# Kernel tuning notes

Hardware: AMD Instinct MI355X
Metric: run time of the kernel (lower is better)

## Reference

```python
import jax, jax.numpy as jnp
import numpy as np

B, S, E, H, R = 8, 1024, 768, 12, 16

def setup_inputs() -> dict:
    key = jax.random.key(0)
    ks = jax.random.split(key, 9)
    sc = 0.02
    return {
        "q": jax.random.normal(ks[0], (B, S, E), jnp.float32),
        "k": jax.random.normal(ks[1], (B, S, E), jnp.float32),
        "v": jax.random.normal(ks[2], (B, S, E), jnp.float32),
        "in_proj_weight": jax.random.normal(ks[3], (3 * E, E), jnp.float32) * sc,
        "in_proj_bias": jax.random.normal(ks[4], (3 * E,), jnp.float32) * sc,
        "out_w": jax.random.normal(ks[5], (E, E), jnp.float32) * sc,
        "out_b": jax.random.normal(ks[6], (E,), jnp.float32) * sc,
        "lora_a": jax.random.normal(ks[7], (R, E), jnp.float32) * sc,
        "lora_b": jax.random.normal(ks[8], (3 * E, R), jnp.float32) * sc,
        "num_heads": H,
    }

def _heads(x, h):
    b, s, e = x.shape
    return x.reshape(b, s, h, e // h).transpose(0, 2, 1, 3)  # [B,H,S,D]

def reference(q, k, v, in_proj_weight, in_proj_bias, out_w, out_b, lora_a, lora_b, num_heads):
    e = q.shape[-1]
    hd = e // num_heads
    scaling = float(hd) ** -0.5
    wq, wk, wv = in_proj_weight[:e], in_proj_weight[e:2 * e], in_proj_weight[2 * e:]
    bq, bk, bv = in_proj_bias[:e], in_proj_bias[e:2 * e], in_proj_bias[2 * e:]
    # base projections + LoRA delta (x @ A^T @ B_slice^T)
    qh = _heads(q @ wq.T + bq + (q @ lora_a.T) @ lora_b[:e].T, num_heads)
    kh = _heads(k @ wk.T + bk + (k @ lora_a.T) @ lora_b[e:2 * e].T, num_heads)
    vh = _heads(v @ wv.T + bv + (v @ lora_a.T) @ lora_b[2 * e:].T, num_heads)
    qh = qh * scaling
    attn = jax.nn.softmax(jnp.einsum('bhqd,bhkd->bhqk', qh, kh), axis=-1)
    out = jnp.einsum('bhqk,bhkd->bhqd', attn, vh)  # [B,H,S,D]
    out = out.transpose(0, 2, 1, 3).reshape(q.shape[0], q.shape[1], e)
    return out @ out_w.T + out_b
```

## Files before the change

kernel.cpp:

```cpp
#include <hip/hip_runtime.h>
#include <hip/hip_bf16.h>


typedef __attribute__((ext_vector_type(4))) float f32x4;
typedef __attribute__((ext_vector_type(16))) float f32x16;
typedef __attribute__((ext_vector_type(8))) short bf16x8;
typedef __attribute__((ext_vector_type(4))) short s16x4;

#define E_DIM 768
#define NB 8
#define SEQ 1024
#define NH 12
#define HD 64
#define M_DIM (NB * SEQ)

__device__ __forceinline__ short f2b(float f) {
    union { __hip_bfloat16 h; short s; } u;
    u.h = __float2bfloat16(f);
    return u.s;
}

__device__ __forceinline__ void async_cp16(const void* g, void* l) {
    __builtin_amdgcn_global_load_lds(
        (const __attribute__((address_space(1))) void*)g,
        (__attribute__((address_space(3))) void*)l, 16, 0, 0);
}


__global__ void cvt_qkv_kernel(const float* __restrict__ q, const float* __restrict__ k,
                               const float* __restrict__ v, short* __restrict__ dst) {
    const float* src = (blockIdx.y == 0) ? q : (blockIdx.y == 1 ? k : v);
    short* out = dst + (size_t)blockIdx.y * (size_t)(M_DIM * E_DIM);
    size_t i = ((size_t)blockIdx.x * 256 + threadIdx.x) * 8;
    float4 a = *(const float4*)(src + i);
    float4 b = *(const float4*)(src + i + 4);
    bf16x8 o;
    o[0] = f2b(a.x); o[1] = f2b(a.y); o[2] = f2b(a.z); o[3] = f2b(a.w);
    o[4] = f2b(b.x); o[5] = f2b(b.y); o[6] = f2b(b.z); o[7] = f2b(b.w);
    *(bf16x8*)(out + i) = o;
}

__global__ void weff_kernel(const float* __restrict__ ipw, const float* __restrict__ la,
                            const float* __restrict__ lb, short* __restrict__ W) {
    int idx = blockIdx.x * 256 + threadIdx.x;
    int r = idx / 192;
    int c = (idx % 192) * 4;
    float4 acc = *(const float4*)(ipw + (size_t)r * E_DIM + c);
    #pragma unroll
    for (int j = 0; j < 16; ++j) {
        float bb = lb[r * 16 + j];
        float4 aa = *(const float4*)(la + j * E_DIM + c);
        acc.x += bb * aa.x; acc.y += bb * aa.y; acc.z += bb * aa.z; acc.w += bb * aa.w;
    }
    s16x4 o; o[0] = f2b(acc.x); o[1] = f2b(acc.y); o[2] = f2b(acc.z); o[3] = f2b(acc.w);
    *(s16x4*)(W + (size_t)r * E_DIM + c) = o;
}

__global__ void cvt_w_kernel(const float* __restrict__ w, short* __restrict__ out) {
    int i = (blockIdx.x * 256 + threadIdx.x) * 4;
    float4 a = *(const float4*)(w + i);
    s16x4 o; o[0] = f2b(a.x); o[1] = f2b(a.y); o[2] = f2b(a.z); o[3] = f2b(a.w);
    *(s16x4*)(out + i) = o;
}

template <int MODE>
__global__ __launch_bounds__(256) void gemm_bt(
    const short* __restrict__ Aall, const short* __restrict__ Ball,
    const float* __restrict__ biasAll,
    short* __restrict__ Qb, short* __restrict__ Kb, short* __restrict__ Vt,
    float* __restrict__ Cout) {
    __shared__ short sA[128 * 64];
    __shared__ short sB[128 * 64];
    const int z = blockIdx.z;
    const short* Ap = Aall + (size_t)z * (size_t)(M_DIM * E_DIM);
    const short* Bp = Ball + (size_t)z * (size_t)(E_DIM * E_DIM);
    const float* bias = biasAll + z * E_DIM;
    const int tm = blockIdx.x * 128;
    const int tn = blockIdx.y * 128;
    const int t = threadIdx.x;
    const int lane = t & 63, wid = t >> 6;
    const int wr = wid >> 1, wc = wid & 1;
    const int lr = lane & 15, lg = lane >> 4;
    const int srow = lane >> 3;
    const int sgrp = lane & 7;

    f32x4 acc[4][4] = {};

    for (int k0 = 0; k0 < E_DIM; k0 += 64) {
        #pragma unroll
        for (int is = 0; is < 4; ++is) {
            const int rbase = is * 32 + wid * 8;
            const int row = rbase + srow;
            const int gsw = (sgrp ^ (row & 7)) << 3;
            async_cp16(Ap + (size_t)(tm + row) * E_DIM + k0 + gsw, &sA[rbase * 64]);
            async_cp16(Bp + (size_t)(tn + row) * E_DIM + k0 + gsw, &sB[rbase * 64]);
        }
        __syncthreads();
        #pragma unroll
        for (int kk = 0; kk < 2; ++kk) {
            bf16x8 af[4], bfr[4];
            const int kg = kk * 4 + lg;
            #pragma unroll
            for (int i = 0; i < 4; ++i) {
                const int row = wr * 64 + i * 16 + lr;
                af[i] = *(const bf16x8*)&sA[row * 64 + ((kg ^ (row & 7)) << 3)];
            }
            #pragma unroll
            for (int j = 0; j < 4; ++j) {
                const int col = wc * 64 + j * 16 + lr;
                bfr[j] = *(const bf16x8*)&sB[col * 64 + ((kg ^ (col & 7)) << 3)];
            }
            #pragma unroll
            for (int i = 0; i < 4; ++i)
                #pragma unroll
                for (int j = 0; j < 4; ++j)
                    acc[i][j] = __builtin_amdgcn_mfma_f32_16x16x32_bf16(
                        af[i], bfr[j], acc[i][j], 0, 0, 0);
        }
        __syncthreads();
    }

    #pragma unroll
    for (int i = 0; i < 4; ++i) {
        const int m0 = tm + wr * 64 + i * 16 + lg * 4;
        const int b = m0 >> 10;
        const int s0 = m0 & 1023;
        #pragma unroll
        for (int j = 0; j < 4; ++j) {
            const int n = tn + wc * 64 + j * 16 + lr;
            const float bia = bias[n];
            f32x4 a = acc[i][j];
            if (MODE == 1) {
                #pragma unroll
                for (int r = 0; r < 4; ++r)
                    Cout[(size_t)(m0 + r) * E_DIM + n] = a[r] + bia;
            } else {
                const int h = n >> 6, d = n & 63;
                const int bh = b * NH + h;
                if (z == 0) {
                    #pragma unroll
                    for (int r = 0; r < 4; ++r)
                        Qb[((size_t)bh * SEQ + s0 + r) * HD + d] = f2b((a[r] + bia) * 0.125f);
                } else if (z == 1) {
                    #pragma unroll
                    for (int r = 0; r < 4; ++r)
                        Kb[((size_t)bh * SEQ + s0 + r) * HD + d] = f2b(a[r] + bia);
                } else {
                    s16x4 pk;
                    #pragma unroll
                    for (int r = 0; r < 4; ++r) pk[r] = f2b(a[r] + bia);
                    *(s16x4*)&Vt[((size_t)bh * HD + d) * SEQ + s0] = pk;
                }
            }
        }
    }
}

__global__ __launch_bounds__(256) void attn_kernel(
    const short* __restrict__ Qb, const short* __restrict__ Kb,
    const short* __restrict__ Vt, short* __restrict__ Ob) {
    __shared__ short sK[2][32 * HD];
    __shared__ short sV[2][HD * 32];

    const int t = threadIdx.x;
    const int lane = t & 63, wid = t >> 6;
    const int l31 = lane & 31, hi = lane >> 5;

    const int p = blockIdx.x;
    const int bh = (p & 7) * 12 + ((p >> 3) >> 3);
    const int qblk = (p >> 3) & 7;
    const int q0 = qblk * 128 + wid * 32;

    const short* Qp = Qb + (size_t)bh * (SEQ * HD);
    const short* Kp = Kb + (size_t)bh * (SEQ * HD);
    const short* Vp = Vt + (size_t)bh * (HD * SEQ);

    bf16x8 qf[4];
    #pragma unroll
    for (int ds = 0; ds < 4; ++ds)
        qf[ds] = *(const bf16x8*)&Qp[(size_t)(q0 + l31) * HD + ds * 16 + hi * 8];

    f32x16 o0 = {}, o1 = {};
    float mr = -1e30f, lsum = 0.f;

    const int kr = wid * 8 + (lane >> 3), kg = lane & 7;
    const int vr = wid * 16 + (lane >> 2), vg = lane & 3;

    int cur = 0;
    async_cp16(Kp + (size_t)kr * HD + 8 * (kg ^ (kr & 7)), &sK[0][wid * 512]);
    async_cp16(Vp + (size_t)vr * SEQ + 8 * (vg ^ ((vr >> 1) & 3)), &sV[0][wid * 512]);
    __syncthreads();

    for (int kb = 0; kb < SEQ; kb += 32) {
        if (kb + 32 < SEQ) {
            async_cp16(Kp + (size_t)(kb + 32 + kr) * HD + 8 * (kg ^ (kr & 7)),
                       &sK[cur ^ 1][wid * 512]);
            async_cp16(Vp + (size_t)vr * SEQ + (kb + 32) + 8 * (vg ^ ((vr >> 1) & 3)),
                       &sV[cur ^ 1][wid * 512]);
        }
        f32x16 st = {};
        #pragma unroll
        for (int ds = 0; ds < 4; ++ds) {
            bf16x8 kf = *(const bf16x8*)&sK[cur][l31 * HD + 8 * ((ds * 2 + hi) ^ (l31 & 7))];
            st = __builtin_amdgcn_mfma_f32_32x32x16_bf16(kf, qf[ds], st, 0, 0, 0);
        }
        float tmax = st[0];
        #pragma unroll
        for (int i = 1; i < 16; ++i) tmax = fmaxf(tmax, st[i]);
        tmax = fmaxf(tmax, __shfl_xor(tmax, 32));
        if (!__all(tmax <= mr + 8.0f)) {
            float mn = fmaxf(mr, tmax);
            float sc = __expf(mr - mn);
            mr = mn;
            lsum *= sc;
            #pragma unroll
            for (int i = 0; i < 16; ++i) { o0[i] *= sc; o1[i] *= sc; }
        }
        float ts = 0.f;
        #pragma unroll
        for (int i = 0; i < 16; ++i) {
            float pv = __expf(st[i] - mr);
            st[i] = pv;
            ts += pv;
        }
        lsum += ts + __shfl_xor(ts, 32);
        bf16x8 pf[2];
        #pragma unroll
        for (int kc = 0; kc < 2; ++kc) {
            const int b0 = kc * 8;
            unsigned w0, w1, w2, w3;
            asm("v_cvt_pk_bf16_f32 %0, %1, %2" : "=v"(w0) : "v"(st[b0 + 0]), "v"(st[b0 + 1]));
            asm("v_cvt_pk_bf16_f32 %0, %1, %2" : "=v"(w1) : "v"(st[b0 + 2]), "v"(st[b0 + 3]));
            asm("v_cvt_pk_bf16_f32 %0, %1, %2" : "=v"(w2) : "v"(st[b0 + 4]), "v"(st[b0 + 5]));
            asm("v_cvt_pk_bf16_f32 %0, %1, %2" : "=v"(w3) : "v"(st[b0 + 6]), "v"(st[b0 + 7]));
            asm("v_permlane32_swap_b32 %0, %1" : "+v"(w0), "+v"(w2));
            asm("v_permlane32_swap_b32 %0, %1" : "+v"(w1), "+v"(w3));
            union { unsigned u[4]; bf16x8 v; } pk;
            pk.u[0] = w0; pk.u[1] = w1; pk.u[2] = w2; pk.u[3] = w3;
            pf[kc] = pk.v;
        }
        #pragma unroll
        for (int kc = 0; kc < 2; ++kc) {
            bf16x8 vf0 = *(const bf16x8*)&sV[cur][l31 * 32 +
                             8 * ((kc * 2 + hi) ^ ((l31 >> 1) & 3))];
            o0 = __builtin_amdgcn_mfma_f32_32x32x16_bf16(vf0, pf[kc], o0, 0, 0, 0);
            const int r1 = l31 + 32;
            bf16x8 vf1 = *(const bf16x8*)&sV[cur][r1 * 32 +
                             8 * ((kc * 2 + hi) ^ ((r1 >> 1) & 3))];
            o1 = __builtin_amdgcn_mfma_f32_32x32x16_bf16(vf1, pf[kc], o1, 0, 0, 0);
        }
        __syncthreads();
        cur ^= 1;
    }

    const int b = bh / NH, h = bh % NH;
    const float inv = 1.0f / lsum;
    short* orow = Ob + (size_t)(b * SEQ + q0 + l31) * E_DIM + h * HD;
    #pragma unroll
    for (int qi = 0; qi < 4; ++qi) {
        s16x4 pk0, pk1;
        #pragma unroll
        for (int r = 0; r < 4; ++r) {
            pk0[r] = f2b(o0[qi * 4 + r] * inv);
            pk1[r] = f2b(o1[qi * 4 + r] * inv);
        }
        *(s16x4*)&orow[qi * 8 + hi * 4]      = pk0;
        *(s16x4*)&orow[32 + qi * 8 + hi * 4] = pk1;
    }
}


extern "C" void kernel_launch(void* const* d_in, const int* in_sizes, int n_in,
                              void* d_out, int out_size, void* d_ws, size_t ws_size,
                              hipStream_t stream) {
    const float* q   = (const float*)d_in[0];
    const float* k   = (const float*)d_in[1];
    const float* v   = (const float*)d_in[2];
    const float* ipw = (const float*)d_in[3];
    const float* ipb = (const float*)d_in[4];
    const float* ow  = (const float*)d_in[5];
    const float* ob  = (const float*)d_in[6];
    const float* la  = (const float*)d_in[7];
    const float* lb  = (const float*)d_in[8];
    float* out = (float*)d_out;

    short* qb   = (short*)d_ws;
    short* weff = qb + (size_t)3 * M_DIM * E_DIM;
    short* oww  = weff + (size_t)2304 * E_DIM;
    short* Qbf  = oww + (size_t)E_DIM * E_DIM;
    short* Kbf  = Qbf + (size_t)M_DIM * E_DIM;
    short* Vtb  = Kbf + (size_t)M_DIM * E_DIM;
    short* Obf  = qb;

    cvt_qkv_kernel<<<dim3(3072, 3), 256, 0, stream>>>(q, k, v, qb);
    weff_kernel<<<1728, 256, 0, stream>>>(ipw, la, lb, weff);
    cvt_w_kernel<<<576, 256, 0, stream>>>(ow, oww);
    gemm_bt<0><<<dim3(64, 6, 3), 256, 0, stream>>>(qb, weff, ipb, Qbf, Kbf, Vtb, nullptr);
    attn_kernel<<<768, 256, 0, stream>>>(Qbf, Kbf, Vtb, Obf);
    gemm_bt<1><<<dim3(64, 6, 1), 256, 0, stream>>>(Obf, oww, ob, nullptr, nullptr, nullptr, out);
}
```

Baseline: 257.7 us.

## Fuse fp32-to-bf16 input conversion into QKV GEMM and double-buffer GEMM tiles

Drops the separate q/k/v bf16 conversion kernel. The QKV GEMM now loads fp32 activations into registers, converts them and writes them to LDS itself. It also adds double-buffered LDS for A and B, so the next k-tile is prefetched while MFMAs run on the current one. The two weight-prep kernels are merged into a single launch. This avoids a full write and re-read of the 3x8Kx768 bf16 activations and one sync per k-step, at the cost of more register pressure and twice the LDS footprint (64KB per block), which may reduce occupancy.

```diff
diff --git a/kernel.cpp b/kernel.cpp
--- a/kernel.cpp
+++ b/kernel.cpp
@@ -13,6 +13,7 @@
 #define NH 12
 #define HD 64
 #define M_DIM (NB * SEQ)
+#define NKT (E_DIM / 64)
 
 __device__ __forceinline__ short f2b(float f) {
     union { __hip_bfloat16 h; short s; } u;
@@ -26,53 +27,41 @@
         (__attribute__((address_space(3))) void*)l, 16, 0, 0);
 }
 
-
-__global__ void cvt_qkv_kernel(const float* __restrict__ q, const float* __restrict__ k,
-                               const float* __restrict__ v, short* __restrict__ dst) {
-    const float* src = (blockIdx.y == 0) ? q : (blockIdx.y == 1 ? k : v);
-    short* out = dst + (size_t)blockIdx.y * (size_t)(M_DIM * E_DIM);
-    size_t i = ((size_t)blockIdx.x * 256 + threadIdx.x) * 8;
-    float4 a = *(const float4*)(src + i);
-    float4 b = *(const float4*)(src + i + 4);
-    bf16x8 o;
-    o[0] = f2b(a.x); o[1] = f2b(a.y); o[2] = f2b(a.z); o[3] = f2b(a.w);
-    o[4] = f2b(b.x); o[5] = f2b(b.y); o[6] = f2b(b.z); o[7] = f2b(b.w);
-    *(bf16x8*)(out + i) = o;
-}
-
-__global__ void weff_kernel(const float* __restrict__ ipw, const float* __restrict__ la,
-                            const float* __restrict__ lb, short* __restrict__ W) {
-    int idx = blockIdx.x * 256 + threadIdx.x;
-    int r = idx / 192;
-    int c = (idx % 192) * 4;
-    float4 acc = *(const float4*)(ipw + (size_t)r * E_DIM + c);
-    #pragma unroll
-    for (int j = 0; j < 16; ++j) {
-        float bb = lb[r * 16 + j];
-        float4 aa = *(const float4*)(la + j * E_DIM + c);
-        acc.x += bb * aa.x; acc.y += bb * aa.y; acc.z += bb * aa.z; acc.w += bb * aa.w;
-    }
-    s16x4 o; o[0] = f2b(acc.x); o[1] = f2b(acc.y); o[2] = f2b(acc.z); o[3] = f2b(acc.w);
-    *(s16x4*)(W + (size_t)r * E_DIM + c) = o;
-}
-
-__global__ void cvt_w_kernel(const float* __restrict__ w, short* __restrict__ out) {
-    int i = (blockIdx.x * 256 + threadIdx.x) * 4;
-    float4 a = *(const float4*)(w + i);
-    s16x4 o; o[0] = f2b(a.x); o[1] = f2b(a.y); o[2] = f2b(a.z); o[3] = f2b(a.w);
-    *(s16x4*)(out + i) = o;
+__global__ void prep_w_kernel(const float* __restrict__ ipw, const float* __restrict__ la,
+                              const float* __restrict__ lb, const float* __restrict__ ow,
+                              short* __restrict__ W, short* __restrict__ OW) {
+    if (blockIdx.x < 1728) {
+        int idx = blockIdx.x * 256 + threadIdx.x;
+        int r = idx / 192;
+        int c = (idx % 192) * 4;
+        float4 acc = *(const float4*)(ipw + (size_t)r * E_DIM + c);
+        #pragma unroll
+        for (int j = 0; j < 16; ++j) {
+            float bb = lb[r * 16 + j];
+            float4 aa = *(const float4*)(la + j * E_DIM + c);
+            acc.x += bb * aa.x; acc.y += bb * aa.y; acc.z += bb * aa.z; acc.w += bb * aa.w;
+        }
+        s16x4 o; o[0] = f2b(acc.x); o[1] = f2b(acc.y); o[2] = f2b(acc.z); o[3] = f2b(acc.w);
+        *(s16x4*)(W + (size_t)r * E_DIM + c) = o;
+    } else {
+        int i = ((blockIdx.x - 1728) * 256 + threadIdx.x) * 4;
+        float4 a = *(const float4*)(ow + i);
+        s16x4 o; o[0] = f2b(a.x); o[1] = f2b(a.y); o[2] = f2b(a.z); o[3] = f2b(a.w);
+        *(s16x4*)(OW + i) = o;
+    }
 }
 
 template <int MODE>
 __global__ __launch_bounds__(256) void gemm_bt(
-    const short* __restrict__ Aall, const short* __restrict__ Ball,
-    const float* __restrict__ biasAll,
+    const float* __restrict__ Aq, const float* __restrict__ Ak,
+    const float* __restrict__ Av, const short* __restrict__ Abf,
+    const short* __restrict__ Ball, const float* __restrict__ biasAll,
     short* __restrict__ Qb, short* __restrict__ Kb, short* __restrict__ Vt,
     float* __restrict__ Cout) {
-    __shared__ short sA[128 * 64];
-    __shared__ short sB[128 * 64];
+    __shared__ short sA[2][128 * 64];
+    __shared__ short sB[2][128 * 64];
     const int z = blockIdx.z;
-    const short* Ap = Aall + (size_t)z * (size_t)(M_DIM * E_DIM);
+    const float* Afp = (MODE == 0) ? (z == 0 ? Aq : (z == 1 ? Ak : Av)) : nullptr;
     const short* Bp = Ball + (size_t)z * (size_t)(E_DIM * E_DIM);
     const float* bias = biasAll + z * E_DIM;
     const int tm = blockIdx.x * 128;
@@ -83,19 +72,62 @@
     const int lr = lane & 15, lg = lane >> 4;
     const int srow = lane >> 3;
     const int sgrp = lane & 7;
-
-    f32x4 acc[4][4] = {};
-
-    for (int k0 = 0; k0 < E_DIM; k0 += 64) {
+    const int arow = t >> 1;
+    const int ahalf = t & 1;
+
+    float4 areg[8];
+
+    auto stageB = [&](short* dst, int k0) {
         #pragma unroll
         for (int is = 0; is < 4; ++is) {
             const int rbase = is * 32 + wid * 8;
             const int row = rbase + srow;
             const int gsw = (sgrp ^ (row & 7)) << 3;
-            async_cp16(Ap + (size_t)(tm + row) * E_DIM + k0 + gsw, &sA[rbase * 64]);
-            async_cp16(Bp + (size_t)(tn + row) * E_DIM + k0 + gsw, &sB[rbase * 64]);
-        }
-        __syncthreads();
+            async_cp16(Bp + (size_t)(tn + row) * E_DIM + k0 + gsw, dst + rbase * 64);
+        }
+    };
+    auto stageA16 = [&](short* dst, int k0) {
+        #pragma unroll
+        for (int is = 0; is < 4; ++is) {
+            const int rbase = is * 32 + wid * 8;
+            const int row = rbase + srow;
+            const int gsw = (sgrp ^ (row & 7)) << 3;
+            async_cp16(Abf + (size_t)(tm + row) * E_DIM + k0 + gsw, dst + rbase * 64);
+        }
+    };
+    auto loadA = [&](int k0) {
+        const float* src = Afp + (size_t)(tm + arow) * E_DIM + k0 + ahalf * 32;
+        #pragma unroll
+        for (int g = 0; g < 8; ++g) areg[g] = ((const float4*)src)[g];
+    };
+    auto writeA = [&](short* dst) {
+        #pragma unroll
+        for (int g = 0; g < 4; ++g) {
+            bf16x8 w;
+            w[0] = f2b(areg[2 * g].x);     w[1] = f2b(areg[2 * g].y);
+            w[2] = f2b(areg[2 * g].z);     w[3] = f2b(areg[2 * g].w);
+            w[4] = f2b(areg[2 * g + 1].x); w[5] = f2b(areg[2 * g + 1].y);
+            w[6] = f2b(areg[2 * g + 1].z); w[7] = f2b(areg[2 * g + 1].w);
+            const int kgrp = ahalf * 4 + g;
+            *(bf16x8*)&dst[arow * 64 + ((kgrp ^ (arow & 7)) << 3)] = w;
+        }
+    };
+
+    f32x4 acc[4][4] = {};
+
+    if (MODE == 0) { loadA(0); stageB(sB[0], 0); writeA(sA[0]); }
+    else           { stageA16(sA[0], 0); stageB(sB[0], 0); }
+    __syncthreads();
+
+    int cur = 0;
+    for (int kt = 0; kt < NKT; ++kt) {
+        const int k0n = (kt + 1) * 64;
+        const bool more = (kt + 1 < NKT);
+        if (more) {
+            stageB(sB[cur ^ 1], k0n);
+            if (MODE == 0) loadA(k0n);
+            else stageA16(sA[cur ^ 1], k0n);
+        }
         #pragma unroll
         for (int kk = 0; kk < 2; ++kk) {
             bf16x8 af[4], bfr[4];
@@ -103,12 +135,12 @@
             #pragma unroll
             for (int i = 0; i < 4; ++i) {
                 const int row = wr * 64 + i * 16 + lr;
-                af[i] = *(const bf16x8*)&sA[row * 64 + ((kg ^ (row & 7)) << 3)];
+                af[i] = *(const bf16x8*)&sA[cur][row * 64 + ((kg ^ (row & 7)) << 3)];
             }
             #pragma unroll
             for (int j = 0; j < 4; ++j) {
                 const int col = wc * 64 + j * 16 + lr;
-                bfr[j] = *(const bf16x8*)&sB[col * 64 + ((kg ^ (col & 7)) << 3)];
+                bfr[j] = *(const bf16x8*)&sB[cur][col * 64 + ((kg ^ (col & 7)) << 3)];
             }
             #pragma unroll
             for (int i = 0; i < 4; ++i)
@@ -117,7 +149,9 @@
                     acc[i][j] = __builtin_amdgcn_mfma_f32_16x16x32_bf16(
                         af[i], bfr[j], acc[i][j], 0, 0, 0);
         }
+        if (MODE == 0 && more) writeA(sA[cur ^ 1]);
         __syncthreads();
+        cur ^= 1;
     }
 
     #pragma unroll
@@ -292,10 +326,10 @@
     short* Vtb  = Kbf + (size_t)M_DIM * E_DIM;
     short* Obf  = qb;
 
-    cvt_qkv_kernel<<<dim3(3072, 3), 256, 0, stream>>>(q, k, v, qb);
-    weff_kernel<<<1728, 256, 0, stream>>>(ipw, la, lb, weff);
-    cvt_w_kernel<<<576, 256, 0, stream>>>(ow, oww);
-    gemm_bt<0><<<dim3(64, 6, 3), 256, 0, stream>>>(qb, weff, ipb, Qbf, Kbf, Vtb, nullptr);
+    prep_w_kernel<<<2304, 256, 0, stream>>>(ipw, la, lb, ow, weff, oww);
+    gemm_bt<0><<<dim3(64, 6, 3), 256, 0, stream>>>(q, k, v, nullptr, weff, ipb,
+                                                   Qbf, Kbf, Vtb, nullptr);
     attn_kernel<<<768, 256, 0, stream>>>(Qbf, Kbf, Vtb, Obf);
-    gemm_bt<1><<<dim3(64, 6, 1), 256, 0, stream>>>(Obf, oww, ob, nullptr, nullptr, nullptr, out);
-}
+    gemm_bt<1><<<dim3(64, 6, 1), 256, 0, stream>>>(nullptr, nullptr, nullptr, Obf,
+                                                   oww, ob, nullptr, nullptr, nullptr, out);
+}
```

Result: slower. 281.6 us (+9.3%).

## Double-buffer GEMM LDS tiles and merge weight prep kernels

Applied to the files above, without the earlier changes.

The bf16 GEMM now keeps two LDS buffers and issues the async global-to-LDS loads for the next k-tile before computing on the current one. It waits with a partial vmcnt so load latency overlaps the MFMA work. The two small weight-preparation kernels are merged into one launch to cut launch overhead. LDS use doubles to 64KB per block, which may lower occupancy, and the vmcnt(8) wait assumes exactly 8 outstanding loads per thread.

```diff
diff --git a/kernel.cpp b/kernel.cpp
--- a/kernel.cpp
+++ b/kernel.cpp
@@ -13,6 +13,7 @@
 #define NH 12
 #define HD 64
 #define M_DIM (NB * SEQ)
+#define NKT (E_DIM / 64)
 
 __device__ __forceinline__ short f2b(float f) {
     union { __hip_bfloat16 h; short s; } u;
@@ -40,27 +41,28 @@
     *(bf16x8*)(out + i) = o;
 }
 
-__global__ void weff_kernel(const float* __restrict__ ipw, const float* __restrict__ la,
-                            const float* __restrict__ lb, short* __restrict__ W) {
-    int idx = blockIdx.x * 256 + threadIdx.x;
-    int r = idx / 192;
-    int c = (idx % 192) * 4;
-    float4 acc = *(const float4*)(ipw + (size_t)r * E_DIM + c);
-    #pragma unroll
-    for (int j = 0; j < 16; ++j) {
-        float bb = lb[r * 16 + j];
-        float4 aa = *(const float4*)(la + j * E_DIM + c);
-        acc.x += bb * aa.x; acc.y += bb * aa.y; acc.z += bb * aa.z; acc.w += bb * aa.w;
-    }
-    s16x4 o; o[0] = f2b(acc.x); o[1] = f2b(acc.y); o[2] = f2b(acc.z); o[3] = f2b(acc.w);
-    *(s16x4*)(W + (size_t)r * E_DIM + c) = o;
-}
-
-__global__ void cvt_w_kernel(const float* __restrict__ w, short* __restrict__ out) {
-    int i = (blockIdx.x * 256 + threadIdx.x) * 4;
-    float4 a = *(const float4*)(w + i);
-    s16x4 o; o[0] = f2b(a.x); o[1] = f2b(a.y); o[2] = f2b(a.z); o[3] = f2b(a.w);
-    *(s16x4*)(out + i) = o;
+__global__ void prep_w_kernel(const float* __restrict__ ipw, const float* __restrict__ la,
+                              const float* __restrict__ lb, const float* __restrict__ ow,
+                              short* __restrict__ W, short* __restrict__ OW) {
+    if (blockIdx.x < 1728) {
+        int idx = blockIdx.x * 256 + threadIdx.x;
+        int r = idx / 192;
+        int c = (idx % 192) * 4;
+        float4 acc = *(const float4*)(ipw + (size_t)r * E_DIM + c);
+        #pragma unroll
+        for (int j = 0; j < 16; ++j) {
+            float bb = lb[r * 16 + j];
+            float4 aa = *(const float4*)(la + j * E_DIM + c);
+            acc.x += bb * aa.x; acc.y += bb * aa.y; acc.z += bb * aa.z; acc.w += bb * aa.w;
+        }
+        s16x4 o; o[0] = f2b(acc.x); o[1] = f2b(acc.y); o[2] = f2b(acc.z); o[3] = f2b(acc.w);
+        *(s16x4*)(W + (size_t)r * E_DIM + c) = o;
+    } else {
+        int i = ((blockIdx.x - 1728) * 256 + threadIdx.x) * 4;
+        float4 a = *(const float4*)(ow + i);
+        s16x4 o; o[0] = f2b(a.x); o[1] = f2b(a.y); o[2] = f2b(a.z); o[3] = f2b(a.w);
+        *(s16x4*)(OW + i) = o;
+    }
 }
 
 template <int MODE>
@@ -69,8 +71,8 @@
     const float* __restrict__ biasAll,
     short* __restrict__ Qb, short* __restrict__ Kb, short* __restrict__ Vt,
     float* __restrict__ Cout) {
-    __shared__ short sA[128 * 64];
-    __shared__ short sB[128 * 64];
+    __shared__ short sA[2][128 * 64];
+    __shared__ short sB[2][128 * 64];
     const int z = blockIdx.z;
     const short* Ap = Aall + (size_t)z * (size_t)(M_DIM * E_DIM);
     const short* Bp = Ball + (size_t)z * (size_t)(E_DIM * E_DIM);
@@ -84,18 +86,30 @@
     const int srow = lane >> 3;
     const int sgrp = lane & 7;
 
-    f32x4 acc[4][4] = {};
-
-    for (int k0 = 0; k0 < E_DIM; k0 += 64) {
+    auto stageAB = [&](short* dA, short* dB, int k0) {
         #pragma unroll
         for (int is = 0; is < 4; ++is) {
             const int rbase = is * 32 + wid * 8;
             const int row = rbase + srow;
             const int gsw = (sgrp ^ (row & 7)) << 3;
-            async_cp16(Ap + (size_t)(tm + row) * E_DIM + k0 + gsw, &sA[rbase * 64]);
-            async_cp16(Bp + (size_t)(tn + row) * E_DIM + k0 + gsw, &sB[rbase * 64]);
-        }
-        __syncthreads();
+            async_cp16(Ap + (size_t)(tm + row) * E_DIM + k0 + gsw, dA + rbase * 64);
+            async_cp16(Bp + (size_t)(tn + row) * E_DIM + k0 + gsw, dB + rbase * 64);
+        }
+    };
+
+    f32x4 acc[4][4] = {};
+
+    stageAB(sA[0], sB[0], 0);
+    int cur = 0;
+    for (int kt = 0; kt < NKT; ++kt) {
+        const bool more = (kt + 1 < NKT);
+        if (more) {
+            stageAB(sA[cur ^ 1], sB[cur ^ 1], (kt + 1) * 64);
+            asm volatile("s_waitcnt vmcnt(8)" ::: "memory");
+        } else {
+            asm volatile("s_waitcnt vmcnt(0)" ::: "memory");
+        }
+        __builtin_amdgcn_s_barrier();
         #pragma unroll
         for (int kk = 0; kk < 2; ++kk) {
             bf16x8 af[4], bfr[4];
@@ -103,12 +117,12 @@
             #pragma unroll
             for (int i = 0; i < 4; ++i) {
                 const int row = wr * 64 + i * 16 + lr;
-                af[i] = *(const bf16x8*)&sA[row * 64 + ((kg ^ (row & 7)) << 3)];
+                af[i] = *(const bf16x8*)&sA[cur][row * 64 + ((kg ^ (row & 7)) << 3)];
             }
             #pragma unroll
             for (int j = 0; j < 4; ++j) {
                 const int col = wc * 64 + j * 16 + lr;
-                bfr[j] = *(const bf16x8*)&sB[col * 64 + ((kg ^ (col & 7)) << 3)];
+                bfr[j] = *(const bf16x8*)&sB[cur][col * 64 + ((kg ^ (col & 7)) << 3)];
             }
             #pragma unroll
             for (int i = 0; i < 4; ++i)
@@ -117,7 +131,8 @@
                     acc[i][j] = __builtin_amdgcn_mfma_f32_16x16x32_bf16(
                         af[i], bfr[j], acc[i][j], 0, 0, 0);
         }
-        __syncthreads();
+        __builtin_amdgcn_s_barrier();
+        cur ^= 1;
     }
 
     #pragma unroll
@@ -293,8 +308,7 @@
     short* Obf  = qb;
 
     cvt_qkv_kernel<<<dim3(3072, 3), 256, 0, stream>>>(q, k, v, qb);
-    weff_kernel<<<1728, 256, 0, stream>>>(ipw, la, lb, weff);
-    cvt_w_kernel<<<576, 256, 0, stream>>>(ow, oww);
+    prep_w_kernel<<<2304, 256, 0, stream>>>(ipw, la, lb, ow, weff, oww);
     gemm_bt<0><<<dim3(64, 6, 3), 256, 0, stream>>>(qb, weff, ipb, Qbf, Kbf, Vtb, nullptr);
     attn_kernel<<<768, 256, 0, stream>>>(Qbf, Kbf, Vtb, Obf);
     gemm_bt<1><<<dim3(64, 6, 1), 256, 0, stream>>>(Obf, oww, ob, nullptr, nullptr, nullptr, out);
```

After: 241.7 us. 1.07x faster.
